# Performance work log

Hardware: AMD Instinct MI355X
Metric: run time of the kernel (lower is better)

Reference implementation:

```python
import jax, jax.numpy as jnp
import numpy as np

# Dims: tokens [B,H,W,C]; 3x3 local window (NB=9 neighbors); relative-pos embed dim RP.
B, H, W, C = 4, 96, 96, 128
K, NB, RP = 3, 9, 8
HID = 128              # edge_hidden_dim = max(hidden_dim//2=128, feature_dim=128)
EDGE_IN = 3 * C + RP   # [center, neighbor, center-neighbor, rel_pos] -> 392
CLIP = 3.0
GATE_EPS = 1e-6
LN_EPS = 1e-5


def _ln(x, w, b):
    m = jnp.mean(x, axis=-1, keepdims=True)
    v = jnp.mean((x - m) ** 2, axis=-1, keepdims=True)
    return (x - m) * jax.lax.rsqrt(v + LN_EPS) * w + b


def _mlp(x, w1, b1, w2, b2):
    # Linear -> GELU (exact/erf, torch default) -> Linear; dropout is identity in eval mode.
    return jax.nn.gelu(x @ w1 + b1, approximate=False) @ w2 + b2


def _eml(drive, resistance, gamma_raw, lam, bias, warmup_eta):
    # EMLUnit energy gate (source not provided; Ohm's-law style drive/resistance,
    # positive resistance via softplus, clipped, warmup-scaled, learned bias).
    gamma = jax.nn.softplus(gamma_raw)
    conduct = drive / (jax.nn.softplus(resistance) + gamma + GATE_EPS)
    return warmup_eta * jnp.clip(lam * conduct, -CLIP, CLIP) + bias


def setup_inputs() -> dict:
    key = jax.random.key(0)
    ks = jax.random.split(key, 8)

    def w(k, shape, std=0.01):
        return jax.random.normal(k, shape, jnp.float32) * std

    return {
        "tokens": jax.random.normal(ks[0], (B, H, W, C), jnp.float32),
        "ln1_w": jnp.ones((C,), jnp.float32), "ln1_b": jnp.zeros((C,), jnp.float32),
        "ln2_w": jnp.ones((C,), jnp.float32), "ln2_b": jnp.zeros((C,), jnp.float32),
        "rel_pos": w(ks[1], (NB, RP), 0.02),
        "d_w1": w(ks[2], (EDGE_IN, HID)), "d_b1": jnp.zeros((HID,), jnp.float32),
        "d_w2": w(ks[3], (HID, 1)), "d_b2": jnp.zeros((1,), jnp.float32),
        "r_w1": w(ks[4], (EDGE_IN, HID)), "r_b1": jnp.zeros((HID,), jnp.float32),
        "r_w2": w(ks[5], (HID, 1)), "r_b2": jnp.zeros((1,), jnp.float32),
        "v_w": w(ks[6], (C, C)), "v_b": jnp.zeros((C,), jnp.float32),
        "o_w": w(ks[7], (C, C)), "o_b": jnp.zeros((C,), jnp.float32),
        "eml_gamma": jnp.full((1,), 0.1, jnp.float32),
        "eml_lam": jnp.ones((1,), jnp.float32),
        "eml_bias": jnp.full((1,), -0.3, jnp.float32),
    }


def reference(tokens, ln1_w, ln1_b, ln2_w, ln2_b, rel_pos,
              d_w1, d_b1, d_w2, d_b2, r_w1, r_b1, r_w2, r_b2,
              v_w, v_b, o_w, o_b, eml_gamma, eml_lam, eml_bias):
    b, h, w_, c = tokens.shape
    hw = h * w_
    norm = _ln(tokens, ln1_w, ln1_b)
    # nn.Unfold(kernel=3, padding=1): zero-pad then gather 3x3 windows (row-major ky,kx order).
    pad = jnp.pad(norm, ((0, 0), (1, 1), (1, 1), (0, 0)))
    neigh = jnp.stack([pad[:, dy:dy + h, dx:dx + w_, :]
                       for dy in range(K) for dx in range(K)], axis=3)  # [B,H,W,9,C]
    neigh = neigh.reshape(b, hw, NB, c)
    center = jnp.broadcast_to(norm.reshape(b, hw, 1, c), (b, hw, NB, c))
    relp = jnp.broadcast_to(rel_pos[None, None], (b, hw, NB, RP))
    edge = jnp.concatenate([center, neigh, center - neigh, relp], axis=-1)  # [B,HW,9,392]
    drive = _mlp(edge, d_w1, d_b1, d_w2, d_b2)[..., 0]        # [B,HW,9]
    resistance = _mlp(edge, r_w1, r_b1, r_w2, r_b2)[..., 0]   # [B,HW,9]
    energy = _eml(drive, resistance, eml_gamma, eml_lam, eml_bias, 1.0)
    gate = jax.nn.sigmoid(energy)[..., None]                  # [B,HW,9,1]
    values = neigh @ v_w + v_b                                # [B,HW,9,C]
    gate_mass = jnp.clip(jnp.sum(gate, axis=2), GATE_EPS, None)  # [B,HW,1]
    message = jnp.sum(gate * values, axis=2) / gate_mass      # [B,HW,C]
    update = (message @ o_w + o_b).reshape(b, h, w_, c)
    return _ln(tokens + update, ln2_w, ln2_b)
```

## Files before the change

kernel.cpp:

```cpp
#include <hip/hip_runtime.h>
#include <stdint.h>

#define NPIX 36864

using bf16x8 = __attribute__((ext_vector_type(8))) short;
using f32x4  = __attribute__((ext_vector_type(4))) float;
using f32x2  = __attribute__((ext_vector_type(2))) float;

__device__ __forceinline__ float bf2f(uint16_t u){
  return __uint_as_float(((uint32_t)u) << 16);
}
__device__ __forceinline__ float bl(uint32_t u){ return __uint_as_float(u << 16); }
__device__ __forceinline__ float bh(uint32_t u){ return __uint_as_float(u & 0xFFFF0000u); }
__device__ __forceinline__ uint16_t f2bf(float f){
  uint32_t u = __float_as_uint(f);
  u += 0x7fffu + ((u >> 16) & 1u);
  return (uint16_t)(u >> 16);
}
__device__ __forceinline__ float ldw(const void* p, int i, bool f32){
  return f32 ? ((const float*)p)[i] : bf2f(((const uint16_t*)p)[i]);
}
__device__ __forceinline__ bool probe_f32(const void* ones_vec){
  return ((const uint32_t*)ones_vec)[0] == 0x3F800000u;
}
__device__ __forceinline__ float softplusf(float x){
  return fmaxf(x, 0.f) + __logf(1.f + __expf(-fabsf(x)));
}
__device__ __forceinline__ f32x2 up2(uint32_t u){
  f32x2 r; r.x = __uint_as_float(u << 16); r.y = __uint_as_float(u & 0xFFFF0000u); return r;
}
__device__ __forceinline__ void sg2(f32x2& acc, uint32_t c, uint32_t n, f32x2 r, f32x2 w){
  f32x2 z = up2(c) + up2(n) + r;
  float sx = __builtin_amdgcn_fmed3f(fmaf(z.x, 0.4255f, 0.5f), 0.f, 1.f);
  float sy = __builtin_amdgcn_fmed3f(fmaf(z.y, 0.4255f, 0.5f), 0.f, 1.f);
  acc.x = fmaf(z.x * sx, w.x, acc.x);
  acc.y = fmaf(z.y * sy, w.y, acc.y);
}

#define LIDX(p, ch) ((p)*128 + ((((ch) >> 3) ^ ((p) & 15)) << 3) + ((ch) & 7))

__global__ __launch_bounds__(256) void pre_kernel(const void* __restrict__ tokens,
                            const void* __restrict__ ln1w, const void* __restrict__ ln1b,
                            const void* __restrict__ dw1, const void* __restrict__ rw1,
                            const void* __restrict__ vw,  const void* __restrict__ relp,
                            const void* __restrict__ db1, const void* __restrict__ rb1,
                            const void* __restrict__ ow,
                            const void* __restrict__ dw2, const void* __restrict__ rw2,
                            const void* __restrict__ vb,  const void* __restrict__ db2,
                            const void* __restrict__ rb2, const void* __restrict__ eg,
                            const void* __restrict__ el,  const void* __restrict__ eb,
                            uint16_t* __restrict__ norm,
                            uint16_t* __restrict__ wcatT, float* __restrict__ Rd,
                            float* __restrict__ Rr, uint16_t* __restrict__ owT,
                            float* __restrict__ w2df, float* __restrict__ w2rf,
                            float* __restrict__ vbf, float* __restrict__ sc){
  const bool F = probe_f32(ln1w);
  const int b = blockIdx.x;
  if (b < NPIX/4){
    const int wv = threadIdx.x >> 6, lane = threadIdx.x & 63;
    const int p = b * 4 + wv;
    float f0, f1;
    if (F){
      const float2 t = ((const float2*)tokens)[(size_t)p*64 + lane];
      f0 = t.x; f1 = t.y;
    } else {
      const uint32_t pk = ((const uint32_t*)tokens)[(size_t)p*64 + lane];
      f0 = bl(pk); f1 = bh(pk);
    }
    float s = f0 + f1;
    #pragma unroll
    for (int m = 1; m < 64; m <<= 1) s += __shfl_xor(s, m, 64);
    const float mean = s * (1.f/128.f);
    const float d0 = f0 - mean, d1 = f1 - mean;
    float q = d0*d0 + d1*d1;
    #pragma unroll
    for (int m = 1; m < 64; m <<= 1) q += __shfl_xor(q, m, 64);
    const float rs = rsqrtf(q * (1.f/128.f) + 1e-5f);
    const float n0 = d0*rs*ldw(ln1w, 2*lane, F)   + ldw(ln1b, 2*lane, F);
    const float n1 = d1*rs*ldw(ln1w, 2*lane+1, F) + ldw(ln1b, 2*lane+1, F);
    ((uint32_t*)(norm + (size_t)p*128))[lane] = (uint32_t)f2bf(n0) | ((uint32_t)f2bf(n1) << 16);
    return;
  }
  const int j = (b - NPIX/4) * 2 + (threadIdx.x >> 7);
  const int c = threadIdx.x & 127;
  if (j < 640){
    float val;
    if (j < 128)      val = ldw(dw1, c*128 + j, F)             + ldw(dw1, (256+c)*128 + j, F);
    else if (j < 256) val = ldw(dw1, (128+c)*128 + (j-128), F) - ldw(dw1, (256+c)*128 + (j-128), F);
    else if (j < 384) val = ldw(rw1, c*128 + (j-256), F)       + ldw(rw1, (256+c)*128 + (j-256), F);
    else if (j < 512) val = ldw(rw1, (128+c)*128 + (j-384), F) - ldw(rw1, (256+c)*128 + (j-384), F);
    else              val = ldw(vw, c*128 + (j-512), F);
    wcatT[j*128 + c] = f2bf(val);
  } else if (j < 649){
    const int k = j - 640;
    float sd = ldw(db1, c, F);
    float sr = ldw(rb1, c, F);
    #pragma unroll
    for (int r = 0; r < 8; ++r){
      float rp = ldw(relp, k*8 + r, F);
      sd += rp * ldw(dw1, (384+r)*128 + c, F);
      sr += rp * ldw(rw1, (384+r)*128 + c, F);
    }
    Rd[k*128 + c] = sd;
    Rr[k*128 + c] = sr;
  } else if (j < 777){
    const int n = j - 649;
    owT[n*128 + c] = f2bf(ldw(ow, c*128 + n, F));
  } else {
    w2df[c] = ldw(dw2, c, F);
    w2rf[c] = ldw(rw2, c, F);
    vbf[c]  = ldw(vb, c, F);
    if (c == 0){
      sc[0] = ldw(db2, 0, F);
      sc[1] = ldw(rb2, 0, F);
      sc[2] = softplusf(ldw(eg, 0, F));
      sc[3] = ldw(el, 0, F);
      sc[4] = ldw(eb, 0, F);
    }
  }
}

__global__ __launch_bounds__(512) void mega_kernel(
    const uint16_t* __restrict__ norm, const uint16_t* __restrict__ wcatT,
    const uint16_t* __restrict__ owT,
    const float* __restrict__ Rd, const float* __restrict__ Rr,
    const float* __restrict__ w2df, const float* __restrict__ w2rf,
    const float* __restrict__ sc, const float* __restrict__ vbf,
    const void* __restrict__ tokens, const void* __restrict__ ob,
    const void* __restrict__ ln2w, const void* __restrict__ ln2b,
    void* __restrict__ out){
  __shared__ __align__(16) char smem[111104];
  uint16_t* const Ns = (uint16_t*)smem;
  uint16_t* const PA = (uint16_t*)(smem + 28672);
  uint16_t* const PB = (uint16_t*)(smem + 57344);
  uint16_t* const Ws = (uint16_t*)(smem + 73728);
  float*    const drv = (float*)(smem + 106496);
  float*    const gts = (float*)(smem + 108800);
  float*    const U   = (float*)smem;

  const int bid0 = blockIdx.x;
  const int bid  = (bid0 & 7)*72 + (bid0 >> 3);
  const int b  = bid / 144;
  const int tl = bid - b*144;
  const int ty = tl / 12;
  const int y0 = ty*8, x0 = (tl - ty*12)*8;
  const int tid = threadIdx.x;
  const int wv = tid >> 6, lane = tid & 63;
  const int lr = lane & 15, quad = lane >> 4;
  const float sc0 = sc[0], sc1 = sc[1], sc2 = sc[2], sc3 = sc[3], sc4 = sc[4];

  #pragma unroll
  for (int i = 0; i < 4; ++i){
    const int idx = tid + i*512;
    if (idx < 1792){
      const int hq = idx >> 4, g = idx & 15;
      uint4 v = {0u,0u,0u,0u};
      if (hq < 100){
        const int hy = hq/10, hx = hq - hy*10;
        const int y = y0 - 1 + hy, x = x0 - 1 + hx;
        if (((unsigned)y < 96u) && ((unsigned)x < 96u))
          v = *(const uint4*)&norm[((size_t)((b*96+y)*96+x))*128 + g*8];
      }
      *(uint4*)&Ns[hq*128 + ((g ^ (hq & 15)) << 3)] = v;
    }
  }

  auto stageW = [&](const uint16_t* __restrict__ src){
    #pragma unroll
    for (int i = 0; i < 4; ++i){
      const int idx = tid + i*512;
      const int r = idx >> 4, g = idx & 15;
      *(uint4*)&Ws[r*128 + ((g ^ (r & 15)) << 3)] = *(const uint4*)&src[(size_t)r*128 + g*8];
    }
  };

  auto gemmH = [&](){
    f32x4 acc[7] = {};
    #pragma unroll
    for (int kk = 0; kk < 4; ++kk){
      const int chunk = kk*4 + quad;
      const bf16x8 bf = *(const bf16x8*)&Ws[(wv*16+lr)*128 + ((chunk ^ lr) << 3)];
      #pragma unroll
      for (int mi = 0; mi < 7; ++mi){
        const int r = mi*16 + lr;
        const bf16x8 a = *(const bf16x8*)&Ns[r*128 + ((chunk ^ (r & 15)) << 3)];
        acc[mi] = __builtin_amdgcn_mfma_f32_16x16x32_bf16(a, bf, acc[mi], 0, 0, 0);
      }
    }
    const int col = wv*16 + lr;
    #pragma unroll
    for (int mi = 0; mi < 7; ++mi){
      const int rowb = mi*16 + quad*4;
      #pragma unroll
      for (int r = 0; r < 4; ++r)
        PA[LIDX(rowb + r, col)] = f2bf(acc[mi][r]);
    }
  };

  auto gemmC = [&](){
    f32x4 acc[4] = {};
    #pragma unroll
    for (int kk = 0; kk < 4; ++kk){
      const int chunk = kk*4 + quad;
      const bf16x8 bf = *(const bf16x8*)&Ws[(wv*16+lr)*128 + ((chunk ^ lr) << 3)];
      #pragma unroll
      for (int mi = 0; mi < 4; ++mi){
        const int r = mi*16 + lr;
        const int hr = (r >> 3)*10 + (r & 7) + 11;
        const bf16x8 a = *(const bf16x8*)&Ns[hr*128 + ((chunk ^ (hr & 15)) << 3)];
        acc[mi] = __builtin_amdgcn_mfma_f32_16x16x32_bf16(a, bf, acc[mi], 0, 0, 0);
      }
    }
    const int col = wv*16 + lr;
    #pragma unroll
    for (int mi = 0; mi < 4; ++mi){
      const int rowb = mi*16 + quad*4;
      #pragma unroll
      for (int r = 0; r < 4; ++r)
        PB[LIDX(rowb + r, col)] = f2bf(acc[mi][r]);
    }
  };

  auto edge = [&](const float* __restrict__ Rk, const float* __restrict__ w2, bool isDrive){
    const int pl = lane >> 3, cg = lane & 7;
    for (int i = 0; i < 9; ++i){
      const int it = wv*9 + i;
      const int k = it >> 3, ry = it & 7;
      const int ky = k/3, kx = k - ky*3;
      const int pr = ry*8 + pl;
      const int hq = (ry + ky)*10 + pl + kx;
      const int g0 = 2*cg;
      const uint4 c0 = *(const uint4*)((const char*)PB + pr*256 + (((g0)  ^ (pr & 15)) << 4));
      const uint4 c1 = *(const uint4*)((const char*)PB + pr*256 + (((g0+1)^ (pr & 15)) << 4));
      const uint4 n0 = *(const uint4*)((const char*)PA + hq*256 + (((g0)  ^ (hq & 15)) << 4));
      const uint4 n1 = *(const uint4*)((const char*)PA + hq*256 + (((g0+1)^ (hq & 15)) << 4));
      const float4* r4 = (const float4*)(Rk + k*128) + cg*4;
      const float4* w4 = (const float4*)w2 + cg*4;
      const float4 Ra = r4[0], Rb = r4[1], Rc = r4[2], Rv = r4[3];
      const float4 Wa = w4[0], Wb = w4[1], Wc = w4[2], Wd = w4[3];
      f32x2 a = {0.f, 0.f};
      sg2(a, c0.x, n0.x, f32x2{Ra.x, Ra.y}, f32x2{Wa.x, Wa.y});
      sg2(a, c0.y, n0.y, f32x2{Ra.z, Ra.w}, f32x2{Wa.z, Wa.w});
      sg2(a, c0.z, n0.z, f32x2{Rb.x, Rb.y}, f32x2{Wb.x, Wb.y});
      sg2(a, c0.w, n0.w, f32x2{Rb.z, Rb.w}, f32x2{Wb.z, Wb.w});
      sg2(a, c1.x, n1.x, f32x2{Rc.x, Rc.y}, f32x2{Wc.x, Wc.y});
      sg2(a, c1.y, n1.y, f32x2{Rc.z, Rc.w}, f32x2{Wc.z, Wc.w});
      sg2(a, c1.z, n1.z, f32x2{Rv.x, Rv.y}, f32x2{Wd.x, Wd.y});
      sg2(a, c1.w, n1.w, f32x2{Rv.z, Rv.w}, f32x2{Wd.z, Wd.w});
      float s = a.x + a.y;
      s += __shfl_xor(s, 1, 64); s += __shfl_xor(s, 2, 64); s += __shfl_xor(s, 4, 64);
      if (cg == 0){
        if (isDrive){
          drv[k*64 + pr] = s;
        } else {
          const float drive  = drv[k*64 + pr] + sc0;
          const float resist = s + sc1;
          const float cond = __fdividef(drive, softplusf(resist) + sc2 + 1e-6f);
          const float en = fminf(fmaxf(sc3 * cond, -3.0f), 3.0f) + sc4;
          const float e = __expf(-en);
          gts[k*64 + pr] = __builtin_amdgcn_rcpf(1.0f + e);
        }
      }
    }
  };

  const uint16_t* const W0 = wcatT;
  const uint16_t* const W1 = wcatT + (size_t)1*128*128;
  const uint16_t* const W2 = wcatT + (size_t)2*128*128;
  const uint16_t* const W3 = wcatT + (size_t)3*128*128;
  const uint16_t* const W4 = wcatT + (size_t)4*128*128;

  stageW(W1); __syncthreads();
  gemmH();    __syncthreads();
  stageW(W0); __syncthreads();
  gemmC();    __syncthreads();
  stageW(W3);
  edge(Rd, w2df, true);
  __syncthreads();
  gemmH();    __syncthreads();
  stageW(W2); __syncthreads();
  gemmC();    __syncthreads();
  stageW(W4);
  edge(Rr, w2rf, false);
  __syncthreads();
  gemmH();    __syncthreads();
  stageW(owT);

  {
    const float2 vb2 = ((const float2*)vbf)[lane];
    const int g = lane >> 2, lb = (lane & 3)*4;
    #pragma unroll
    for (int j = 0; j < 8; ++j){
      const int mp = wv*8 + j;
      const int my = mp >> 3, mx = mp & 7;
      float gk[9], gsum = 0.f;
      #pragma unroll
      for (int kk = 0; kk < 9; ++kk){ gk[kk] = gts[kk*64 + mp]; gsum += gk[kk]; }
      float a0 = 0.f, a1 = 0.f;
      #pragma unroll
      for (int kk = 0; kk < 9; ++kk){
        const int kyy = kk / 3;
        const int h2  = (my + kyy)*10 + (mx + kk - kyy*3);
        const uint32_t u = *(const uint32_t*)((const char*)PA + h2*256 + ((g ^ (h2 & 15)) << 4) + lb);
        a0 = fmaf(gk[kk], bl(u), a0);
        a1 = fmaf(gk[kk], bh(u), a1);
      }
      const float inv = __fdividef(1.0f, fmaxf(gsum, 1e-6f));
      a0 = (a0 + gsum * vb2.x) * inv;
      a1 = (a1 + gsum * vb2.y) * inv;
      *(uint32_t*)((char*)PB + mp*256 + ((g ^ (mp & 15)) << 4) + lb) =
          (uint32_t)f2bf(a0) | ((uint32_t)f2bf(a1) << 16);
    }
  }
  __syncthreads();

  f32x4 acc[4] = {};
  #pragma unroll
  for (int kk = 0; kk < 4; ++kk){
    const int chunk = kk*4 + quad;
    const bf16x8 bf = *(const bf16x8*)&Ws[(wv*16+lr)*128 + ((chunk ^ lr) << 3)];
    #pragma unroll
    for (int mi = 0; mi < 4; ++mi){
      const int r = mi*16 + lr;
      const bf16x8 a = *(const bf16x8*)&PB[r*128 + ((chunk ^ (r & 15)) << 3)];
      acc[mi] = __builtin_amdgcn_mfma_f32_16x16x32_bf16(a, bf, acc[mi], 0, 0, 0);
    }
  }
  __syncthreads();
  {
    const int col = wv*16 + lr;
    #pragma unroll
    for (int mi = 0; mi < 4; ++mi)
      #pragma unroll
      for (int r = 0; r < 4; ++r)
        U[(mi*16 + quad*4 + r)*128 + col] = acc[mi][r];
  }
  __syncthreads();

  const bool F = probe_f32(ln2w);
  const float lw0 = ldw(ln2w, 2*lane, F), lw1 = ldw(ln2w, 2*lane+1, F);
  const float lb0 = ldw(ln2b, 2*lane, F), lb1 = ldw(ln2b, 2*lane+1, F);
  const float ob0 = ldw(ob, 2*lane, F),   ob1 = ldw(ob, 2*lane+1, F);
  #pragma unroll
  for (int j = 0; j < 8; ++j){
    const int row = wv*8 + j;
    const int my = row >> 3, mx = row & 7;
    const size_t p = (size_t)((b*96 + y0 + my)*96 + (x0 + mx));
    const float2 uv = ((const float2*)U)[row*64 + lane];
    float t0, t1;
    if (F){
      const float2 tk = ((const float2*)tokens)[p*64 + lane];
      t0 = tk.x; t1 = tk.y;
    } else {
      const uint32_t tk = ((const uint32_t*)tokens)[p*64 + lane];
      t0 = bl(tk); t1 = bh(tk);
    }
    const float a0 = uv.x + ob0 + t0;
    const float a1 = uv.y + ob1 + t1;
    float s = a0 + a1;
    #pragma unroll
    for (int m = 1; m < 64; m <<= 1) s += __shfl_xor(s, m, 64);
    const float mean = s * (1.f/128.f);
    const float d0 = a0 - mean, d1 = a1 - mean;
    float q = d0*d0 + d1*d1;
    #pragma unroll
    for (int m = 1; m < 64; m <<= 1) q += __shfl_xor(q, m, 64);
    const float rs = rsqrtf(q * (1.f/128.f) + 1e-5f);
    const float o0 = d0*rs*lw0 + lb0;
    const float o1 = d1*rs*lw1 + lb1;
    if (F){
      ((float2*)out)[p*64 + lane] = make_float2(o0, o1);
    } else {
      ((uint32_t*)out)[p*64 + lane] = (uint32_t)f2bf(o0) | ((uint32_t)f2bf(o1) << 16);
    }
  }
}

extern "C" void kernel_launch(void* const* d_in, const int* in_sizes, int n_in,
                              void* d_out, int out_size, void* d_ws, size_t ws_size,
                              hipStream_t stream) {
  const void* tokens = d_in[0];
  const void* ln1w   = d_in[1];
  const void* ln1b   = d_in[2];
  const void* ln2w   = d_in[3];
  const void* ln2b   = d_in[4];
  const void* relp   = d_in[5];
  const void* dw1    = d_in[6];
  const void* db1    = d_in[7];
  const void* dw2    = d_in[8];
  const void* db2    = d_in[9];
  const void* rw1    = d_in[10];
  const void* rb1    = d_in[11];
  const void* rw2    = d_in[12];
  const void* rb2    = d_in[13];
  const void* vw     = d_in[14];
  const void* vb     = d_in[15];
  const void* ow     = d_in[16];
  const void* ob     = d_in[17];
  const void* eg     = d_in[18];
  const void* el     = d_in[19];
  const void* eb     = d_in[20];

  char* ws = (char*)d_ws;
  uint16_t* normb = (uint16_t*)(ws + 0);
  uint16_t* wcatT = (uint16_t*)(ws + 9437184);
  float*    Rd    = (float*)   (ws + 9601024);
  float*    Rr    = (float*)   (ws + 9605632);
  uint16_t* owT   = (uint16_t*)(ws + 9610240);
  float*    w2df  = (float*)   (ws + 9643008);
  float*    w2rf  = (float*)   (ws + 9643520);
  float*    vbf   = (float*)   (ws + 9644032);
  float*    sc    = (float*)   (ws + 9644544);

  pre_kernel<<<NPIX/4 + 389, 256, 0, stream>>>(tokens, ln1w, ln1b,
                                       dw1, rw1, vw, relp, db1, rb1, ow,
                                       dw2, rw2, vb, db2, rb2, eg, el, eb,
                                       normb, wcatT, Rd, Rr, owT, w2df, w2rf, vbf, sc);
  mega_kernel<<<576, 512, 0, stream>>>(normb, wcatT, owT, Rd, Rr, w2df, w2rf,
                                       sc, vbf, tokens, ob, ln2w, ln2b, d_out);
}
```

Baseline: 204.3 us.

## Load GEMM weight fragments directly from global into registers, drop LDS weight staging

Removes the shared-memory weight buffer and its staging passes. Each wave now loads its B-operand fragments straight from global memory (L2-resident) into registers before each GEMM. This cuts several block-wide barriers, and the lower LDS footprint lets more blocks share a CU; the launch bounds now request that. The cost is uncoalesced per-lane global loads of weights with exposed latency, and possible register pressure under the tighter launch bound.

```diff
diff --git a/kernel.cpp b/kernel.cpp
--- a/kernel.cpp
+++ b/kernel.cpp
@@ -120,7 +120,7 @@
   }
 }
 
-__global__ __launch_bounds__(512) void mega_kernel(
+__global__ __launch_bounds__(512, 4) void mega_kernel(
     const uint16_t* __restrict__ norm, const uint16_t* __restrict__ wcatT,
     const uint16_t* __restrict__ owT,
     const float* __restrict__ Rd, const float* __restrict__ Rr,
@@ -129,13 +129,12 @@
     const void* __restrict__ tokens, const void* __restrict__ ob,
     const void* __restrict__ ln2w, const void* __restrict__ ln2b,
     void* __restrict__ out){
-  __shared__ __align__(16) char smem[111104];
+  __shared__ __align__(16) char smem[78336];
   uint16_t* const Ns = (uint16_t*)smem;
   uint16_t* const PA = (uint16_t*)(smem + 28672);
   uint16_t* const PB = (uint16_t*)(smem + 57344);
-  uint16_t* const Ws = (uint16_t*)(smem + 73728);
-  float*    const drv = (float*)(smem + 106496);
-  float*    const gts = (float*)(smem + 108800);
+  float*    const drv = (float*)(smem + 73728);
+  float*    const gts = (float*)(smem + 76032);
   float*    const U   = (float*)smem;
 
   const int bid0 = blockIdx.x;
@@ -165,26 +164,25 @@
     }
   }
 
-  auto stageW = [&](const uint16_t* __restrict__ src){
-    #pragma unroll
-    for (int i = 0; i < 4; ++i){
-      const int idx = tid + i*512;
-      const int r = idx >> 4, g = idx & 15;
-      *(uint4*)&Ws[r*128 + ((g ^ (r & 15)) << 3)] = *(const uint4*)&src[(size_t)r*128 + g*8];
-    }
+  auto loadB = [&](const uint16_t* __restrict__ Wp, bf16x8 (&bfr)[4]){
+    const uint16_t* base = Wp + (size_t)(wv*16 + lr)*128 + quad*8;
+    #pragma unroll
+    for (int kk = 0; kk < 4; ++kk)
+      bfr[kk] = *(const bf16x8*)(base + kk*32);
   };
 
-  auto gemmH = [&](){
+  auto gemmH = [&](const uint16_t* __restrict__ Wp){
+    bf16x8 bfr[4];
+    loadB(Wp, bfr);
     f32x4 acc[7] = {};
     #pragma unroll
     for (int kk = 0; kk < 4; ++kk){
       const int chunk = kk*4 + quad;
-      const bf16x8 bf = *(const bf16x8*)&Ws[(wv*16+lr)*128 + ((chunk ^ lr) << 3)];
       #pragma unroll
       for (int mi = 0; mi < 7; ++mi){
         const int r = mi*16 + lr;
         const bf16x8 a = *(const bf16x8*)&Ns[r*128 + ((chunk ^ (r & 15)) << 3)];
-        acc[mi] = __builtin_amdgcn_mfma_f32_16x16x32_bf16(a, bf, acc[mi], 0, 0, 0);
+        acc[mi] = __builtin_amdgcn_mfma_f32_16x16x32_bf16(a, bfr[kk], acc[mi], 0, 0, 0);
       }
     }
     const int col = wv*16 + lr;
@@ -197,18 +195,19 @@
     }
   };
 
-  auto gemmC = [&](){
+  auto gemmC = [&](const uint16_t* __restrict__ Wp){
+    bf16x8 bfr[4];
+    loadB(Wp, bfr);
     f32x4 acc[4] = {};
     #pragma unroll
     for (int kk = 0; kk < 4; ++kk){
       const int chunk = kk*4 + quad;
-      const bf16x8 bf = *(const bf16x8*)&Ws[(wv*16+lr)*128 + ((chunk ^ lr) << 3)];
       #pragma unroll
       for (int mi = 0; mi < 4; ++mi){
         const int r = mi*16 + lr;
         const int hr = (r >> 3)*10 + (r & 7) + 11;
         const bf16x8 a = *(const bf16x8*)&Ns[hr*128 + ((chunk ^ (hr & 15)) << 3)];
-        acc[mi] = __builtin_amdgcn_mfma_f32_16x16x32_bf16(a, bf, acc[mi], 0, 0, 0);
+        acc[mi] = __builtin_amdgcn_mfma_f32_16x16x32_bf16(a, bfr[kk], acc[mi], 0, 0, 0);
       }
     }
     const int col = wv*16 + lr;
@@ -270,21 +269,17 @@
   const uint16_t* const W3 = wcatT + (size_t)3*128*128;
   const uint16_t* const W4 = wcatT + (size_t)4*128*128;
 
-  stageW(W1); __syncthreads();
-  gemmH();    __syncthreads();
-  stageW(W0); __syncthreads();
-  gemmC();    __syncthreads();
-  stageW(W3);
+  __syncthreads();
+  gemmH(W1); gemmC(W0);
+  __syncthreads();
   edge(Rd, w2df, true);
   __syncthreads();
-  gemmH();    __syncthreads();
-  stageW(W2); __syncthreads();
-  gemmC();    __syncthreads();
-  stageW(W4);
+  gemmH(W3); gemmC(W2);
+  __syncthreads();
   edge(Rr, w2rf, false);
   __syncthreads();
-  gemmH();    __syncthreads();
-  stageW(owT);
+  gemmH(W4);
+  __syncthreads();
 
   {
     const float2 vb2 = ((const float2*)vbf)[lane];
@@ -315,15 +310,18 @@
   __syncthreads();
 
   f32x4 acc[4] = {};
-  #pragma unroll
-  for (int kk = 0; kk < 4; ++kk){
-    const int chunk = kk*4 + quad;
-    const bf16x8 bf = *(const bf16x8*)&Ws[(wv*16+lr)*128 + ((chunk ^ lr) << 3)];
-    #pragma unroll
-    for (int mi = 0; mi < 4; ++mi){
-      const int r = mi*16 + lr;
-      const bf16x8 a = *(const bf16x8*)&PB[r*128 + ((chunk ^ (r & 15)) << 3)];
-      acc[mi] = __builtin_amdgcn_mfma_f32_16x16x32_bf16(a, bf, acc[mi], 0, 0, 0);
+  {
+    bf16x8 bfr[4];
+    loadB(owT, bfr);
+    #pragma unroll
+    for (int kk = 0; kk < 4; ++kk){
+      const int chunk = kk*4 + quad;
+      #pragma unroll
+      for (int mi = 0; mi < 4; ++mi){
+        const int r = mi*16 + lr;
+        const bf16x8 a = *(const bf16x8*)&PB[r*128 + ((chunk ^ (r & 15)) << 3)];
+        acc[mi] = __builtin_amdgcn_mfma_f32_16x16x32_bf16(a, bfr[kk], acc[mi], 0, 0, 0);
+      }
     }
   }
   __syncthreads();
```

After: 187.5 us. 1.09x faster.
